# Performance work log

Measured on AMD Instinct MI355X. Metric: run time of the kernel, lower is better.

The kernel has to match this reference:

```python
import jax, jax.numpy as jnp
import numpy as np

NEG = -1e9  # large negative used as log(0) to keep grads finite
EPS = 1e-38


def _pcfg_inside(theta_log, Phi):
    # theta_log: [N,N,N] (A -> B C), Phi: [B,N,T] log terminal probs
    B, N, T = Phi.shape
    tm = jnp.max(theta_log)
    et = jnp.exp(theta_log - tm)  # [A,Bn,Cn], all > 0
    beta = jnp.full((B, N, T, T), NEG, dtype=Phi.dtype)
    idx = jnp.arange(T)
    beta = beta.at[:, :, idx, idx].set(Phi)  # length-1 spans
    for l in range(2, T + 1):
        P = T - l + 1
        ii = jnp.arange(P)
        ss = jnp.arange(l - 1)
        lcol = ii[:, None] + ss[None, :]          # left child end  [P,S]
        left = beta[:, :, ii[:, None], lcol]      # [B,N,P,S]
        right = beta[:, :, lcol + 1, (ii + l - 1)[:, None]]  # [B,N,P,S]
        ml = jnp.max(left, axis=1)                # [B,P,S]
        mr = jnp.max(right, axis=1)
        el = jnp.exp(left - ml[:, None])
        er = jnp.exp(right - mr[:, None])
        inner = jnp.einsum('xyz,byps,bzps->bxps', et, el, er)
        sc = jnp.log(jnp.maximum(inner, EPS)) + tm + ml[:, None] + mr[:, None]
        score = jax.scipy.special.logsumexp(sc, axis=-1)  # over split points -> [B,N,P]
        beta = beta.at[:, :, ii, ii + l - 1].set(score)
    logZ = beta[:, 0, 0, T - 1]  # start symbol id 0, full span
    return beta, logZ


def _pcfg_outside(theta_log, beta):
    B, N, T, _ = beta.shape
    tm = jnp.max(theta_log)
    et = jnp.exp(theta_log - tm)
    alpha = jnp.full((B, N, T, T), NEG, dtype=beta.dtype)
    alpha = alpha.at[:, 0, 0, T - 1].set(0.0)
    for l in range(T, 1, -1):  # parent spans, longest first
        P = T - l + 1
        ii = jnp.arange(P)
        jj = ii + l - 1
        ss = jnp.arange(l - 1)
        lcol = ii[:, None] + ss[None, :]          # left child end  [P,S]
        rrow = lcol + 1                            # right child start
        a = alpha[:, :, ii, jj]                    # [B,N,P]
        lb = beta[:, :, ii[:, None], lcol]         # [B,N,P,S]
        rb = beta[:, :, rrow, jj[:, None]]         # [B,N,P,S]
        ma = jnp.max(a, axis=1)                    # [B,P]
        ea = jnp.exp(a - ma[:, None])
        mrb = jnp.max(rb, axis=1)
        erb = jnp.exp(rb - mrb[:, None])
        mlb = jnp.max(lb, axis=1)
        elb = jnp.exp(lb - mlb[:, None])
        cL = jnp.log(jnp.maximum(jnp.einsum('xyz,bxp,bzps->byps', et, ea, erb), EPS)) \
             + tm + ma[:, None, :, None] + mrb[:, None]
        cR = jnp.log(jnp.maximum(jnp.einsum('xyz,bxp,byps->bzps', et, ea, elb), EPS)) \
             + tm + ma[:, None, :, None] + mlb[:, None]
        alpha = alpha.at[:, :, ii[:, None], lcol].set(
            jnp.logaddexp(alpha[:, :, ii[:, None], lcol], cL))
        alpha = alpha.at[:, :, rrow, jj[:, None]].set(
            jnp.logaddexp(alpha[:, :, rrow, jj[:, None]], cR))
    return alpha


def setup_inputs() -> dict:
    key = jax.random.key(0)
    ks = jax.random.split(key, 6)
    B, T, k, N, V = 16, 32, 512, 24, 32000
    g_seq = jax.random.normal(ks[0], (B, T, k), dtype=jnp.float32)
    Theta = jax.random.normal(ks[1], (N, N, N), dtype=jnp.float32) * 0.01
    nt2vocab = (jax.random.uniform(ks[2], (N, V), dtype=jnp.float32) < 0.05).astype(jnp.float32)
    ln_gamma = jnp.ones((k,), jnp.float32)
    ln_beta = jnp.zeros((k,), jnp.float32)
    W1 = jax.random.normal(ks[3], (k, 128), dtype=jnp.float32) * 0.02
    b1 = jnp.zeros((128,), jnp.float32)
    W2 = jax.random.normal(ks[4], (128, N), dtype=jnp.float32) * 0.02
    b2 = jnp.zeros((N,), jnp.float32)
    return {"g_seq": g_seq, "Theta": Theta, "nt2vocab": nt2vocab,
            "ln_gamma": ln_gamma, "ln_beta": ln_beta,
            "W1": W1, "b1": b1, "W2": W2, "b2": b2}


def reference(g_seq, Theta, nt2vocab, ln_gamma, ln_beta, W1, b1, W2, b2):
    # term head: LayerNorm -> Linear(k,128) -> GELU(exact) -> Linear(128,N)
    mu = jnp.mean(g_seq, axis=-1, keepdims=True)
    var = jnp.var(g_seq, axis=-1, keepdims=True)  # biased, as torch LayerNorm
    g = (g_seq - mu) / jnp.sqrt(var + 1e-5) * ln_gamma + ln_beta
    h = jax.nn.gelu(g @ W1 + b1, approximate=False)
    out = h @ W2 + b2                                # [B,T,N]
    Phi = jax.nn.log_softmax(out.transpose(0, 2, 1), axis=1)   # [B,N,T]
    theta_log = jax.nn.log_softmax(Theta, axis=-1)   # softmax over flattened (B,C) last dim == axis -1 of [N,N,N] after view(-1,N)
    N = Theta.shape[0]
    theta_log = jax.nn.log_softmax(Theta.reshape(-1, N), axis=-1).reshape(N, N, N)
    beta, logZ = _pcfg_inside(theta_log, Phi)
    alpha = _pcfg_outside(theta_log, beta)
    T = Phi.shape[2]
    idx = jnp.arange(T)
    p_nt = jnp.exp(alpha[:, :, idx, idx] + beta[:, :, idx, idx] - logZ[:, None, None])  # [B,N,T]
    mask_logits = jnp.log(1e-6 + jnp.einsum('bnt,nv->btv', p_nt, nt2vocab))
    L_pcfg = (-logZ).mean()
    return mask_logits, L_pcfg
```

## Files before the change

kernel.cpp:

```cpp
#include <hip/hip_runtime.h>
#include <math.h>

#define NEGV -1000000000.0f
#define EPSV 1e-38f

constexpr int BSTRIDE = 528 * 32;
constexpr int ASTRIDE = 528 * 24;

__device__ __forceinline__ int tri(int i, int j) { return ((j * (j + 1)) >> 1) + i; }
__device__ __forceinline__ float la2(float a, float c) {
  float mx = fmaxf(a, c), mn = fminf(a, c);
  return mx + log1pf(__expf(mn - mx));
}
__device__ __forceinline__ void gstore(float* p, float v) {
  __hip_atomic_store(p, v, __ATOMIC_RELAXED, __HIP_MEMORY_SCOPE_AGENT);
}
__device__ __forceinline__ float gload(const float* p) {
  return __hip_atomic_load(p, __ATOMIC_RELAXED, __HIP_MEMORY_SCOPE_AGENT);
}
__device__ __forceinline__ void storeu(unsigned* p, unsigned v) {
  __hip_atomic_store(p, v, __ATOMIC_RELAXED, __HIP_MEMORY_SCOPE_AGENT);
}
__device__ __forceinline__ unsigned loadu(const unsigned* p) {
  return __hip_atomic_load(p, __ATOMIC_RELAXED, __HIP_MEMORY_SCOPE_AGENT);
}

__global__ void __launch_bounds__(256, 2) mega_kernel(
    const float* __restrict__ g_seq, const float* __restrict__ Theta,
    const float* __restrict__ vocab, const float* __restrict__ lng,
    const float* __restrict__ lnb, const float* __restrict__ W1,
    const float* __restrict__ bb1, const float* __restrict__ W2,
    const float* __restrict__ bb2, float* __restrict__ out,
    float* __restrict__ et_g, float* __restrict__ beta_g,
    float* __restrict__ aL_g, float* __restrict__ aR_g,
    unsigned* __restrict__ cnt, float* __restrict__ logZg) {
  __shared__ __align__(16) float sm[16160];
  float* etL = sm;
  float* wk = sm + 13824;
  const int tid = threadIdx.x;
  const int blk = blockIdx.x;
  const int b = blk & 15, local = blk >> 4;
  unsigned* gcnt  = cnt;
  unsigned* done  = cnt + 8;
  unsigned* ibc   = cnt + 16 + b * 16;
  unsigned* slots = cnt + 512 + b * 64;
  unsigned* go    = slots + 32;
  float* bbase = beta_g + b * BSTRIDE;
  float* aLb = aL_g + b * ASTRIDE;
  float* aRb = aR_g + b * ASTRIDE;

  {
    float* g = wk;
    float2* red = (float2*)(wk + 512);
    float* hb = wk + 1024;
    float* ob = wk + 1152;
    float* sc = wk + 1184;
    float2 raw = ((const float2*)(g_seq + (size_t)blk * 512))[tid];
    red[tid] = make_float2(raw.x + raw.y, raw.x * raw.x + raw.y * raw.y);
    __syncthreads();
    if (tid < 128) { float2 o = red[tid + 128], m = red[tid]; red[tid] = make_float2(m.x + o.x, m.y + o.y); }
    __syncthreads();
    if (tid < 64) {
      float2 v = red[tid], o = red[tid + 64];
      v.x += o.x; v.y += o.y;
      for (int off = 32; off; off >>= 1) { v.x += __shfl_xor(v.x, off); v.y += __shfl_xor(v.y, off); }
      if (tid == 0) {
        float mu = v.x / 512.0f;
        float var = v.y / 512.0f - mu * mu;
        sc[0] = mu; sc[1] = rsqrtf(var + 1e-5f);
      }
    }
    __syncthreads();
    float mu = sc[0], rstd = sc[1];
    g[2 * tid]     = (raw.x - mu) * rstd * lng[2 * tid]     + lnb[2 * tid];
    g[2 * tid + 1] = (raw.y - mu) * rstd * lng[2 * tid + 1] + lnb[2 * tid + 1];
    __syncthreads();
    {
      int j = tid & 127, hh = tid >> 7, c0 = hh * 256;
      float a0 = 0, a1 = 0, a2 = 0, a3 = 0;
      for (int c = 0; c < 256; c += 4) {
        a0 = fmaf(g[c0 + c],     W1[(c0 + c) * 128 + j],     a0);
        a1 = fmaf(g[c0 + c + 1], W1[(c0 + c + 1) * 128 + j], a1);
        a2 = fmaf(g[c0 + c + 2], W1[(c0 + c + 2) * 128 + j], a2);
        a3 = fmaf(g[c0 + c + 3], W1[(c0 + c + 3) * 128 + j], a3);
      }
      ((float*)red)[tid] = (a0 + a1) + (a2 + a3);
    }
    __syncthreads();
    if (tid < 128) {
      float a = ((float*)red)[tid] + ((float*)red)[tid + 128] + bb1[tid];
      hb[tid] = 0.5f * a * (1.0f + erff(a * 0.70710678118654752f));
    }
    __syncthreads();
    if (tid < 192) {
      int n = tid >> 3, q = tid & 7;
      float a = 0;
      for (int k = 0; k < 16; k++) a = fmaf(hb[q * 16 + k], W2[(q * 16 + k) * 24 + n], a);
      ((float*)red)[tid] = a;
    }
    __syncthreads();
    if (tid < 24) {
      float a = bb2[tid];
      for (int q = 0; q < 8; q++) a += ((float*)red)[tid * 8 + q];
      ob[tid] = a;
    }
    __syncthreads();
    if (tid == 0) {
      float m = ob[0];
      for (int n = 1; n < 24; n++) m = fmaxf(m, ob[n]);
      float s = 0;
      for (int n = 0; n < 24; n++) s += __expf(ob[n] - m);
      sc[2] = m + __logf(s);
    }
    __syncthreads();
    if (tid < 24) {
      int fb = blk >> 5, ft = blk & 31;
      gstore(beta_g + (size_t)fb * BSTRIDE + tri(ft, ft) * 32 + tid, ob[tid] - sc[2]);
    }
  }
  if (tid < 64) {
    int z = tid & 31;
    bool up = tid >= 32;
    int row = up ? (512 + blk) : blk;
    bool valid = (!up) || (blk < 64);
    float v = (z < 24 && valid) ? Theta[row * 24 + z] : NEGV;
    float m = v;
    for (int off = 16; off; off >>= 1) m = fmaxf(m, __shfl_xor(m, off));
    float e = (z < 24 && valid) ? __expf(v - m) : 0.f;
    float s = e;
    for (int off = 16; off; off >>= 1) s += __shfl_xor(s, off);
    float lse = m + __logf(s);
    if (z < 24 && valid) gstore(et_g + row * 24 + z, __expf(v - lse));
  }
  for (int idx = blk * 256 + tid; idx < 2 * 16 * ASTRIDE; idx += 131072) {
    float v = NEGV;
    if (idx < 16 * ASTRIDE && (idx % ASTRIDE) == 11904) v = 0.f;
    gstore(aL_g + idx, v);
  }
  __builtin_amdgcn_s_waitcnt(0);
  __syncthreads();
  if (tid == 0) {
    __hip_atomic_fetch_add(ibc, 1u, __ATOMIC_RELAXED, __HIP_MEMORY_SCOPE_AGENT);
    if (local == 0) {
      while (loadu(ibc) < 32u) __builtin_amdgcn_s_sleep(2);
      __hip_atomic_fetch_add(gcnt, 1u, __ATOMIC_RELAXED, __HIP_MEMORY_SCOPE_AGENT);
    }
    while (loadu(gcnt) < 16u) __builtin_amdgcn_s_sleep(2);
  }
  __syncthreads();

  for (int i4 = tid; i4 < 3456; i4 += 256)
    ((float4*)etL)[i4] = ((const float4*)et_g)[i4];
  __syncthreads();

  {
    float* eA = wk;
    float* eB = wk + 744;
    float* rr = wk + 1488;
    float* red2 = wk + 2064;
    float* mrl = wk + 2256;
    float* msm = wk + 2288;
    float* scal = wk + 2320;
    for (int l = 2; l <= 32; l++) {
      unsigned e = (unsigned)(l - 1);
      int S = l - 1, P = 33 - l;
      if (tid == 0) { while (loadu(go) < e - 1) __builtin_amdgcn_s_sleep(1); }
      __syncthreads();
      if (local < P) {
        int i = local, j = i + S, SN = S * 24;
        for (int idx4 = tid; idx4 < 6 * S; idx4 += 256) {
          int s = idx4 / 6, q = idx4 - 6 * s;
          ((float4*)eA)[idx4] = ((const float4*)(bbase + (size_t)tri(i, i + s) * 32))[q];
          ((float4*)eB)[idx4] = ((const float4*)(bbase + (size_t)tri(i + s + 1, j) * 32))[q];
        }
        __syncthreads();
        if (tid < 8 * S) {
          int s = tid >> 3, q = tid & 7, y0 = q * 3;
          float pa = fmaxf(fmaxf(eA[s * 24 + y0], eA[s * 24 + y0 + 1]), eA[s * 24 + y0 + 2]);
          float pb = fmaxf(fmaxf(eB[s * 24 + y0], eB[s * 24 + y0 + 1]), eB[s * 24 + y0 + 2]);
          for (int off = 4; off; off >>= 1) {
            pa = fmaxf(pa, __shfl_xor(pa, off));
            pb = fmaxf(pb, __shfl_xor(pb, off));
          }
          if (q == 0) { mrl[s] = pb; msm[s] = pa + pb; }
        }
        __syncthreads();
        if (tid < 32) {
          float v = (tid < S) ? msm[tid] : NEGV;
          for (int off = 16; off; off >>= 1) v = fmaxf(v, __shfl_xor(v, off));
          if (tid == 0) scal[0] = v;
        }
        __syncthreads();
        float M = scal[0];
        for (int idx = tid; idx < SN; idx += 256) {
          int s = idx / 24;
          float m_ = mrl[s];
          eA[idx] = __expf(eA[idx] + m_ - M);
          eB[idx] = __expf(eB[idx] - m_);
        }
        __syncthreads();
        if (tid < 144) {
          int y = tid / 6, zq = tid % 6;
          float4 acc = make_float4(0, 0, 0, 0);
          for (int s = 0; s < S; s++) {
            float a = eA[s * 24 + y];
            float4 b4 = ((float4*)eB)[s * 6 + zq];
            acc.x = fmaf(a, b4.x, acc.x); acc.y = fmaf(a, b4.y, acc.y);
            acc.z = fmaf(a, b4.z, acc.z); acc.w = fmaf(a, b4.w, acc.w);
          }
          ((float4*)rr)[y * 6 + zq] = acc;
        }
        __syncthreads();
        if (tid < 192) {
          int x = tid >> 3, c = tid & 7;
          const float4* e4 = (const float4*)(etL + x * 576 + c * 72);
          const float4* r4 = (const float4*)(rr + c * 72);
          float a0 = 0, a1 = 0;
#pragma unroll
          for (int q = 0; q < 18; q += 2) {
            float4 ev = e4[q], rv = r4[q];
            a0 = fmaf(ev.x, rv.x, fmaf(ev.y, rv.y, fmaf(ev.z, rv.z, fmaf(ev.w, rv.w, a0))));
            float4 e2 = e4[q + 1], r2 = r4[q + 1];
            a1 = fmaf(e2.x, r2.x, fmaf(e2.y, r2.y, fmaf(e2.z, r2.z, fmaf(e2.w, r2.w, a1))));
          }
          red2[tid] = a0 + a1;
        }
        __syncthreads();
        if (tid < 24) {
          float a = 0;
          for (int q = 0; q < 8; q++) a += red2[tid * 8 + q];
          gstore(bbase + (size_t)tri(i, j) * 32 + tid, M + __logf(fmaxf(a, EPSV)));
        }
      }
      __builtin_amdgcn_s_waitcnt(0);
      __syncthreads();
      if (tid == 0) storeu(slots + local, e);
      if (local == 0 && tid < 64) {
        for (;;) {
          unsigned v = e;
          if (tid < 32) v = loadu(slots + tid);
          if (__ballot(v >= e) == ~0ull) break;
          __builtin_amdgcn_s_sleep(1);
        }
        if (tid == 0) storeu(go, e);
      }
    }
  }
  if (local == 0 && tid == 0) {
    gstore(logZg + b, gload(bbase + 496 * 32));
    __hip_atomic_fetch_add(done, 1u, __ATOMIC_RELAXED, __HIP_MEMORY_SCOPE_AGENT);
  }

  {
    float* w = wk;
    float* ebL = wk + 576;
    float* ebR = wk + 1320;
    float* mLs = wk + 2064;
    float* mRs = wk + 2096;
    float* ea24 = wk + 2128;
    float* scal = wk + 2320;
    for (int l = 32; l >= 2; l--) {
      unsigned e = (unsigned)(64 - l);
      int S = l - 1, P = 33 - l;
      if (tid == 0) { while (loadu(go) < e - 1) __builtin_amdgcn_s_sleep(1); }
      __syncthreads();
      if (local < P) {
        int i = local, j = i + S, SN = S * 24;
        if (tid < 32) {
          float av = NEGV;
          if (tid < 24) av = la2(gload(aLb + tri(i, j) * 24 + tid), gload(aRb + tri(i, j) * 24 + tid));
          float m = av;
          for (int off = 16; off; off >>= 1) m = fmaxf(m, __shfl_xor(m, off));
          if (tid < 24) ea24[tid] = __expf(av - m);
          if (tid == 0) scal[0] = m;
        }
        __syncthreads();
        float ma = scal[0];
        if (tid < 144) {
          int y = tid / 6, zq = tid % 6;
          float4 acc = make_float4(0, 0, 0, 0);
#pragma unroll 4
          for (int x = 0; x < 24; x++) {
            float a = ea24[x];
            float4 ev = ((const float4*)(etL + x * 576 + y * 24))[zq];
            acc.x = fmaf(a, ev.x, acc.x); acc.y = fmaf(a, ev.y, acc.y);
            acc.z = fmaf(a, ev.z, acc.z); acc.w = fmaf(a, ev.w, acc.w);
          }
          ((float4*)w)[y * 6 + zq] = acc;
        }
        for (int idx4 = tid; idx4 < 6 * S; idx4 += 256) {
          int s = idx4 / 6, q = idx4 - 6 * s;
          ((float4*)ebL)[idx4] = ((const float4*)(bbase + (size_t)tri(i, i + s) * 32))[q];
          ((float4*)ebR)[idx4] = ((const float4*)(bbase + (size_t)tri(i + s + 1, j) * 32))[q];
        }
        __syncthreads();
        if (tid < 8 * S) {
          int s = tid >> 3, q = tid & 7, y0 = q * 3;
          float pl = fmaxf(fmaxf(ebL[s * 24 + y0], ebL[s * 24 + y0 + 1]), ebL[s * 24 + y0 + 2]);
          float pr = fmaxf(fmaxf(ebR[s * 24 + y0], ebR[s * 24 + y0 + 1]), ebR[s * 24 + y0 + 2]);
          for (int off = 4; off; off >>= 1) {
            pl = fmaxf(pl, __shfl_xor(pl, off));
            pr = fmaxf(pr, __shfl_xor(pr, off));
          }
          if (q == 0) { mLs[s] = pl; mRs[s] = pr; }
        }
        __syncthreads();
        for (int idx = tid; idx < SN; idx += 256) {
          int s = idx / 24;
          ebL[idx] = __expf(ebL[idx] - mLs[s]);
          ebR[idx] = __expf(ebR[idx] - mRs[s]);
        }
        __syncthreads();
        for (int u = tid; u < 2 * SN; u += 256) {
          if (u < SN) {
            int s = u / 24, y = u - s * 24;
            const float4* w4 = (const float4*)(w + y * 24);
            const float4* r4 = (const float4*)(ebR + s * 24);
            float acc = 0;
#pragma unroll
            for (int q = 0; q < 6; q++) {
              float4 a = w4[q], c4 = r4[q];
              acc = fmaf(a.x, c4.x, fmaf(a.y, c4.y, fmaf(a.z, c4.z, fmaf(a.w, c4.w, acc))));
            }
            float val = __logf(fmaxf(acc, EPSV)) + ma + mRs[s];
            float* t = aLb + tri(i, i + s) * 24 + y;
            gstore(t, la2(gload(t), val));
          } else {
            int u2 = u - SN;
            int s = u2 / 24, z = u2 - s * 24;
            float acc = 0;
            for (int y = 0; y < 24; y++) acc = fmaf(w[y * 24 + z], ebL[s * 24 + y], acc);
            float val = __logf(fmaxf(acc, EPSV)) + ma + mLs[s];
            float* t = aRb + tri(i + s + 1, j) * 24 + z;
            gstore(t, la2(gload(t), val));
          }
        }
      }
      __builtin_amdgcn_s_waitcnt(0);
      __syncthreads();
      if (tid == 0) storeu(slots + local, e);
      if (local == 0 && tid < 64) {
        for (;;) {
          unsigned v = e;
          if (tid < 32) v = loadu(slots + tid);
          if (__ballot(v >= e) == ~0ull) break;
          __builtin_amdgcn_s_sleep(1);
        }
        if (tid == 0) storeu(go, e);
      }
    }
  }
  if (tid == 0) { while (loadu(go) < 62u) __builtin_amdgcn_s_sleep(1); }
  __syncthreads();

  {
    float* p = wk;
    float logZv = gload(bbase + 496 * 32);
    for (int c = tid; c < 768; c += 256) {
      int n = c >> 5, t = c & 31;
      int dA = tri(t, t) * 24 + n;
      float al = gload(aLb + dA), ar = gload(aRb + dA);
      p[c] = __expf(la2(al, ar) + bbase[(size_t)tri(t, t) * 32 + n] - logZv);
    }
    __syncthreads();
    int vbase = local * 1000;
    for (int pass = 0; pass < 2; pass++) {
      int o0 = tid + pass * 512, o1 = o0 + 256;
      bool v0ok = o0 < 1000, v1ok = o1 < 1000;
      int v0 = vbase + o0, v1 = vbase + o1;
      float vr0[24], vr1[24];
#pragma unroll
      for (int n = 0; n < 24; n++) {
        vr0[n] = v0ok ? vocab[n * 32000 + v0] : 0.f;
        vr1[n] = v1ok ? vocab[n * 32000 + v1] : 0.f;
      }
      float* ob0 = out + (size_t)b * 32 * 32000 + v0;
      float* ob1 = out + (size_t)b * 32 * 32000 + v1;
      for (int t4 = 0; t4 < 32; t4 += 4) {
        float a00 = 1e-6f, a01 = 1e-6f, a02 = 1e-6f, a03 = 1e-6f;
        float a10 = 1e-6f, a11 = 1e-6f, a12 = 1e-6f, a13 = 1e-6f;
#pragma unroll 6
        for (int n = 0; n < 24; n++) {
          float4 pv = *(const float4*)(p + n * 32 + t4);
          a00 = fmaf(pv.x, vr0[n], a00); a01 = fmaf(pv.y, vr0[n], a01);
          a02 = fmaf(pv.z, vr0[n], a02); a03 = fmaf(pv.w, vr0[n], a03);
          a10 = fmaf(pv.x, vr1[n], a10); a11 = fmaf(pv.y, vr1[n], a11);
          a12 = fmaf(pv.z, vr1[n], a12); a13 = fmaf(pv.w, vr1[n], a13);
        }
        if (v0ok) {
          ob0[(size_t)(t4 + 0) * 32000] = __logf(a00);
          ob0[(size_t)(t4 + 1) * 32000] = __logf(a01);
          ob0[(size_t)(t4 + 2) * 32000] = __logf(a02);
          ob0[(size_t)(t4 + 3) * 32000] = __logf(a03);
        }
        if (v1ok) {
          ob1[(size_t)(t4 + 0) * 32000] = __logf(a10);
          ob1[(size_t)(t4 + 1) * 32000] = __logf(a11);
          ob1[(size_t)(t4 + 2) * 32000] = __logf(a12);
          ob1[(size_t)(t4 + 3) * 32000] = __logf(a13);
        }
      }
    }
    if (blk == 0 && tid == 0) {
      while (loadu(done) < 16u) __builtin_amdgcn_s_sleep(2);
      float s = 0;
      for (int q = 0; q < 16; q++) s += gload(logZg + q);
      out[16384000] = -s / 16.0f;
    }
  }
}

extern "C" void kernel_launch(void* const* d_in, const int* in_sizes, int n_in,
                              void* d_out, int out_size, void* d_ws, size_t ws_size,
                              hipStream_t stream) {
  (void)in_sizes; (void)n_in; (void)out_size; (void)ws_size;
  const float* g_seq = (const float*)d_in[0];
  const float* Theta = (const float*)d_in[1];
  const float* vocab = (const float*)d_in[2];
  const float* lng   = (const float*)d_in[3];
  const float* lnb   = (const float*)d_in[4];
  const float* W1    = (const float*)d_in[5];
  const float* bb1   = (const float*)d_in[6];
  const float* W2    = (const float*)d_in[7];
  const float* bb2   = (const float*)d_in[8];
  float* out = (float*)d_out;

  float* ws = (float*)d_ws;
  unsigned* cnt = (unsigned*)d_ws;
  float* logZg  = ws + 2048;
  float* et_g   = ws + 4096;
  float* beta_g = ws + 18432;
  float* aL_g   = beta_g + 16 * BSTRIDE;
  float* aR_g   = aL_g + 16 * ASTRIDE;

  hipMemsetAsync(d_ws, 0, 8192, stream);

  void* args[] = {(void*)&g_seq, (void*)&Theta, (void*)&vocab, (void*)&lng,
                  (void*)&lnb, (void*)&W1, (void*)&bb1, (void*)&W2, (void*)&bb2,
                  (void*)&out, (void*)&et_g, (void*)&beta_g, (void*)&aL_g,
                  (void*)&aR_g, (void*)&cnt, (void*)&logZg};
  hipLaunchCooperativeKernel((const void*)mega_kernel, dim3(512), dim3(256),
                             args, 0, stream);
}
```

Measured before the change: 501.4 us.

## Replace per-level global barriers with neighbor-to-neighbor wavefront dependencies

The inside and outside dynamic programs no longer sync all 32 span blocks through a leader-driven barrier at every span length. Each block now waits only on its adjacent block's progress counter (local+1 for inside, local-1 for outside); transitivity covers the needed child or parent spans. Each block also stops looping once its span start is out of range. This removes the serialized all-block barrier and lets levels overlap as a wavefront, at the cost of subtler memory-ordering assumptions between relaxed atomic flags and data stores.

```diff
diff --git a/kernel.cpp b/kernel.cpp
--- a/kernel.cpp
+++ b/kernel.cpp
@@ -43,8 +43,8 @@
   unsigned* gcnt  = cnt;
   unsigned* done  = cnt + 8;
   unsigned* ibc   = cnt + 16 + b * 16;
-  unsigned* slots = cnt + 512 + b * 64;
-  unsigned* go    = slots + 32;
+  unsigned* slotI = cnt + 512 + b * 64;
+  unsigned* slotO = slotI + 32;
   float* bbase = beta_g + b * BSTRIDE;
   float* aLb = aL_g + b * ASTRIDE;
   float* aRb = aR_g + b * ASTRIDE;
@@ -161,12 +161,15 @@
     float* mrl = wk + 2256;
     float* msm = wk + 2288;
     float* scal = wk + 2320;
-    for (int l = 2; l <= 32; l++) {
-      unsigned e = (unsigned)(l - 1);
-      int S = l - 1, P = 33 - l;
-      if (tid == 0) { while (loadu(go) < e - 1) __builtin_amdgcn_s_sleep(1); }
+    const int lastLI = 32 - local;
+    for (int l = 2; l <= lastLI; l++) {
+      int S = l - 1;
+      if (l >= 3 && tid == 0) {
+        unsigned need = (unsigned)(l - 1);
+        while (loadu(slotI + local + 1) < need) __builtin_amdgcn_s_sleep(1);
+      }
       __syncthreads();
-      if (local < P) {
+      {
         int i = local, j = i + S, SN = S * 24;
         for (int idx4 = tid; idx4 < 6 * S; idx4 += 256) {
           int s = idx4 / 6, q = idx4 - 6 * s;
@@ -234,16 +237,7 @@
       }
       __builtin_amdgcn_s_waitcnt(0);
       __syncthreads();
-      if (tid == 0) storeu(slots + local, e);
-      if (local == 0 && tid < 64) {
-        for (;;) {
-          unsigned v = e;
-          if (tid < 32) v = loadu(slots + tid);
-          if (__ballot(v >= e) == ~0ull) break;
-          __builtin_amdgcn_s_sleep(1);
-        }
-        if (tid == 0) storeu(go, e);
-      }
+      if (tid == 0) storeu(slotI + local, (unsigned)l);
     }
   }
   if (local == 0 && tid == 0) {
@@ -259,12 +253,15 @@
     float* mRs = wk + 2096;
     float* ea24 = wk + 2128;
     float* scal = wk + 2320;
-    for (int l = 32; l >= 2; l--) {
-      unsigned e = (unsigned)(64 - l);
-      int S = l - 1, P = 33 - l;
-      if (tid == 0) { while (loadu(go) < e - 1) __builtin_amdgcn_s_sleep(1); }
+    const int lastLO = 32 - local;
+    for (int l = lastLO; l >= 2; l--) {
+      int S = l - 1;
+      if (local > 0 && tid == 0) {
+        unsigned need = (unsigned)(32 - l);
+        while (loadu(slotO + local - 1) < need) __builtin_amdgcn_s_sleep(1);
+      }
       __syncthreads();
-      if (local < P) {
+      {
         int i = local, j = i + S, SN = S * 24;
         if (tid < 32) {
           float av = NEGV;
@@ -338,19 +335,17 @@
       }
       __builtin_amdgcn_s_waitcnt(0);
       __syncthreads();
-      if (tid == 0) storeu(slots + local, e);
-      if (local == 0 && tid < 64) {
-        for (;;) {
-          unsigned v = e;
-          if (tid < 32) v = loadu(slots + tid);
-          if (__ballot(v >= e) == ~0ull) break;
-          __builtin_amdgcn_s_sleep(1);
-        }
-        if (tid == 0) storeu(go, e);
-      }
-    }
-  }
-  if (tid == 0) { while (loadu(go) < 62u) __builtin_amdgcn_s_sleep(1); }
+      if (tid == 0) storeu(slotO + local, (unsigned)(33 - l));
+    }
+  }
+  if (tid < 64) {
+    for (;;) {
+      unsigned v = 31;
+      if (tid < 31) v = loadu(slotO + tid);
+      if (__ballot(v >= 31u) == ~0ull) break;
+      __builtin_amdgcn_s_sleep(1);
+    }
+  }
   __syncthreads();
 
   {
```

New measurement: 495.1 us. About the same (-1.3%).
